# Kernel optimization log

Measured on AMD Instinct MI355X. Metric: run time of the kernel, lower is better.

The kernel has to match this reference:

```python
import jax, jax.numpy as jnp
import numpy as np

B, T, D = 2, 4096, 512
H = 8
HD = D // H  # 64


def setup_inputs() -> dict:
    key = jax.random.key(0)
    k1, k2, k3 = jax.random.split(key, 3)
    x = jax.random.normal(k1, (B, T, D), dtype=jnp.float32)
    w_qkv = jax.random.normal(k2, (3 * D, D), dtype=jnp.float32) * (1.0 / np.sqrt(D))
    w_out = jax.random.normal(k3, (D, D), dtype=jnp.float32) * (1.0 / np.sqrt(D))
    return {"x": x, "w_qkv": w_qkv, "w_out": w_out}


def reference(x, w_qkv, w_out):
    b, t, d = x.shape
    qkv = x @ w_qkv.T                      # [B,T,3D]
    q, k, v = jnp.split(qkv, 3, axis=-1)
    # b t (h d) -> b h t d
    def split_heads(a):
        return a.reshape(b, t, H, HD).transpose(0, 2, 1, 3)
    q, k, v = split_heads(q), split_heads(k), split_heads(v)
    scale = 1.0 / np.sqrt(HD).astype(np.float32)
    scores = jnp.einsum('bhqd,bhkd->bhqk', q, k) * scale  # [B,H,T,T]
    causal = jnp.tril(jnp.ones((t, t), dtype=bool))        # keep lower triangle
    scores = jnp.where(causal[None, None], scores, -jnp.inf)
    attn = jax.nn.softmax(scores, axis=-1)
    out = jnp.einsum('bhqk,bhkd->bhqd', attn, v)           # [B,H,T,HD]
    out = out.transpose(0, 2, 1, 3).reshape(b, t, d)       # b h t d -> b t (h d)
    return out @ w_out.T
```

## Files before the change

kernel.cpp:

```cpp
#include <hip/hip_runtime.h>
#include <hip/hip_bf16.h>

#define BB 2
#define TT 4096
#define DD 512
#define HH 8
#define HD 64
#define M_TOT (BB*TT)
#define N_QKV (3*DD)

typedef __attribute__((ext_vector_type(8))) __bf16 bf16x8;
typedef __attribute__((ext_vector_type(4))) float f32x4;

#define MFMA32(a,b,c) __builtin_amdgcn_mfma_f32_16x16x32_bf16((a),(b),(c),0,0,0)

#define SCALE_L2E 0.18033688011112443f
#define SHIFT_L2E 11.541560327111707f

static __device__ __forceinline__ unsigned short f2bf(float f) {
    union { float f; unsigned u; } v; v.f = f;
    return (unsigned short)((v.u + 0x8000u) >> 16);
}
static __device__ __forceinline__ unsigned short f2bf_t(float f) {
    union { float f; unsigned u; } v; v.f = f;
    return (unsigned short)(v.u >> 16);
}

static __device__ __forceinline__ bf16x8 load8(const unsigned short* p) {
    bf16x8 v;
    __builtin_memcpy(&v, p, 16);
    return v;
}

static __device__ __forceinline__ bf16x8 ones_frag() {
    unsigned short u[8];
    #pragma unroll
    for (int i = 0; i < 8; i++) u[i] = 0x3F80;
    bf16x8 v; __builtin_memcpy(&v, u, 16);
    return v;
}

#define GLDS(gp, lp) __builtin_amdgcn_global_load_lds( \
    (const __attribute__((address_space(1))) unsigned int*)(gp), \
    (__attribute__((address_space(3))) unsigned int*)(lp), 16, 0, 0)

#define NX4 (M_TOT*DD/4)
#define NW4 (N_QKV*DD/4)
#define NO4 (DD*DD/4)
__global__ __launch_bounds__(256) void cast_all(
        const float* __restrict__ x, const float* __restrict__ wqkv,
        const float* __restrict__ wout,
        unsigned short* __restrict__ xb, unsigned short* __restrict__ wqkvb,
        unsigned short* __restrict__ woutb) {
    int i = blockIdx.x * 256 + threadIdx.x;
    const float* s; unsigned short* d; int j;
    if (i < NX4)            { s = x;    d = xb;    j = i; }
    else if (i < NX4 + NW4) { s = wqkv; d = wqkvb; j = i - NX4; }
    else                    { s = wout; d = woutb; j = i - NX4 - NW4; }
    float4 f = ((const float4*)s)[j];
    ushort4 o;
    o.x = f2bf(f.x); o.y = f2bf(f.y); o.z = f2bf(f.z); o.w = f2bf(f.w);
    ((ushort4*)d)[j] = o;
}

__global__ __launch_bounds__(256) void qkv_gemm(
        const unsigned short* __restrict__ xb,
        const unsigned short* __restrict__ wb,
        unsigned short* __restrict__ qb,
        unsigned short* __restrict__ kb,
        unsigned short* __restrict__ vtb) {
    __shared__ union {
        struct { unsigned short As[128 * 32]; unsigned short Bs[128 * 32]; } g;
        unsigned short vt[4][64][72];
    } sm;
    int tid = threadIdx.x;
    int w = tid >> 6, lane = tid & 63;
    int lrow = lane & 15, quad = lane >> 4;
    int bn = blockIdx.x % (N_QKV / 128);
    int bm = blockIdx.x / (N_QKV / 128);
    int m0 = bm * 128, n0 = bn * 128;
    int wm = w >> 1, wn = w & 1;

    f32x4 c[4][4];
    #pragma unroll
    for (int i = 0; i < 4; i++)
        #pragma unroll
        for (int j = 0; j < 4; j++) c[i][j] = (f32x4){0.f, 0.f, 0.f, 0.f};

    for (int k0 = 0; k0 < DD; k0 += 32) {
        #pragma unroll
        for (int j = 0; j < 2; j++) {
            int ch = j * 256 + tid;
            int row = ch >> 2, kc = ch & 3;
            GLDS(xb + (size_t)(m0 + row) * DD + k0 + kc * 8,
                 (char*)sm.g.As + (size_t)(j * 256 + w * 64) * 16);
        }
        #pragma unroll
        for (int j = 0; j < 2; j++) {
            int ch = j * 256 + tid;
            int row = ch >> 2, kc = ch & 3;
            GLDS(wb + (size_t)(n0 + row) * DD + k0 + kc * 8,
                 (char*)sm.g.Bs + (size_t)(j * 256 + w * 64) * 16);
        }
        __syncthreads();
        bf16x8 a[4], b[4];
        #pragma unroll
        for (int mf = 0; mf < 4; mf++) a[mf] = load8(&sm.g.As[(wm * 64 + mf * 16 + lrow) * 32 + quad * 8]);
        #pragma unroll
        for (int nf = 0; nf < 4; nf++) b[nf] = load8(&sm.g.Bs[(wn * 64 + nf * 16 + lrow) * 32 + quad * 8]);
        #pragma unroll
        for (int mf = 0; mf < 4; mf++)
            #pragma unroll
            for (int nf = 0; nf < 4; nf++)
                c[mf][nf] = MFMA32(a[mf], b[nf], c[mf][nf]);
        __syncthreads();
    }

    int m0w = m0 + wm * 64, n0w = n0 + wn * 64;
    int which = n0w >> 9;
    int h = (n0w & 511) >> 6;
    if (which < 2) {
        unsigned short* dst = (which == 0) ? qb : kb;
        #pragma unroll
        for (int mf = 0; mf < 4; mf++) {
            #pragma unroll
            for (int r = 0; r < 4; r++) {
                int m = m0w + mf * 16 + quad * 4 + r;
                int t = m & (TT - 1), bi = m >> 12;
                size_t hb = (size_t)(bi * HH + h) * TT + t;
                #pragma unroll
                for (int nf = 0; nf < 4; nf++)
                    dst[hb * HD + nf * 16 + lrow] = f2bf(c[mf][nf][r]);
            }
        }
    } else {
        #pragma unroll
        for (int mf = 0; mf < 4; mf++)
            #pragma unroll
            for (int r = 0; r < 4; r++)
                #pragma unroll
                for (int nf = 0; nf < 4; nf++)
                    sm.vt[w][nf * 16 + lrow][mf * 16 + quad * 4 + r] = f2bf(c[mf][nf][r]);
        int bi = m0w >> 12, t0 = m0w & (TT - 1);
        size_t hb = (size_t)(bi * HH + h) * HD;
        #pragma unroll
        for (int i = 0; i < 8; i++) {
            int d = i * 8 + (lane >> 3);
            int tc = (lane & 7) * 8;
            bf16x8 v;
            __builtin_memcpy(&v, &sm.vt[w][d][tc], 16);
            __builtin_memcpy(vtb + (hb + d) * TT + t0 + tc, &v, 16);
        }
    }
}

__global__ __launch_bounds__(256) void attn_kernel(
        const unsigned short* __restrict__ qb,
        const unsigned short* __restrict__ kb,
        const unsigned short* __restrict__ vtb,
        unsigned short* __restrict__ attnb) {
    __shared__ union {
        unsigned short p[4][64][68];
        float c[2][64][66];
    } sm;

    const f32x4 ZERO4 = {0.f, 0.f, 0.f, 0.f};
    int w = threadIdx.x >> 6;
    int lane = threadIdx.x & 63;
    int lrow = lane & 15, quad = lane >> 4;
    int bh = blockIdx.x & 15;
    int pr = blockIdx.x >> 4;
    int bi = bh >> 3, h = bh & 7;

    const unsigned short* qh = qb + (size_t)bh * TT * HD;
    const unsigned short* kh = kb + (size_t)bh * TT * HD;
    const unsigned short* vth = vtb + (size_t)bh * HD * TT;
    bf16x8 ones = ones_frag();

    for (int half = 0; half < 2; half++) {
        int qt = half ? (63 - pr) : pr;
        int q0 = qt * 64;

        bf16x8 qf[4][2];
        #pragma unroll
        for (int mf = 0; mf < 4; mf++) {
            const unsigned short* qp = qh + (q0 + mf * 16 + lrow) * HD + quad * 8;
            qf[mf][0] = load8(qp);
            qf[mf][1] = load8(qp + 32);
        }

        f32x4 o[4][4];
        f32x4 l[4];
        #pragma unroll
        for (int i = 0; i < 4; i++) {
            l[i] = ZERO4;
            #pragma unroll
            for (int j = 0; j < 4; j++) o[i][j] = ZERO4;
        }

        for (int kt = w; kt <= qt; kt += 4) {
            int kbase = kt * 64;
            bool diag = (kt == qt);
            bf16x8 kf[4][2], vf[4][2];
            #pragma unroll
            for (int nf = 0; nf < 4; nf++) {
                const unsigned short* kp = kh + (kbase + nf * 16 + lrow) * HD + quad * 8;
                kf[nf][0] = load8(kp);
                kf[nf][1] = load8(kp + 32);
                const unsigned short* vp = vth + (nf * 16 + lrow) * TT + kbase + quad * 8;
                vf[nf][0] = load8(vp);
                vf[nf][1] = load8(vp + 32);
            }
            #pragma unroll
            for (int mf = 0; mf < 4; mf++) {
                #pragma unroll
                for (int nf = 0; nf < 4; nf++) {
                    if (diag && nf > mf) {
                        #pragma unroll
                        for (int r = 0; r < 4; r++)
                            sm.p[w][mf * 16 + quad * 4 + r][nf * 16 + lrow] = 0;
                    } else {
                        f32x4 s = MFMA32(qf[mf][0], kf[nf][0], ZERO4);
                        s = MFMA32(qf[mf][1], kf[nf][1], s);
                        #pragma unroll
                        for (int r = 0; r < 4; r++) {
                            float p = __builtin_amdgcn_exp2f(s[r] * SCALE_L2E - SHIFT_L2E);
                            if (diag && nf == mf && lrow > quad * 4 + r) p = 0.f;
                            sm.p[w][mf * 16 + quad * 4 + r][nf * 16 + lrow] = f2bf_t(p);
                        }
                    }
                }
                bf16x8 pa0, pa1;
                __builtin_memcpy(&pa0, &sm.p[w][mf * 16 + lrow][quad * 8], 16);
                __builtin_memcpy(&pa1, &sm.p[w][mf * 16 + lrow][32 + quad * 8], 16);
                l[mf] = MFMA32(pa0, ones, l[mf]);
                l[mf] = MFMA32(pa1, ones, l[mf]);
                #pragma unroll
                for (int nfd = 0; nfd < 4; nfd++) {
                    o[mf][nfd] = MFMA32(pa0, vf[nfd][0], o[mf][nfd]);
                    o[mf][nfd] = MFMA32(pa1, vf[nfd][1], o[mf][nfd]);
                }
            }
        }

        __syncthreads();
        if (w >= 2) {
            int cb = w - 2;
            #pragma unroll
            for (int mf = 0; mf < 4; mf++)
                #pragma unroll
                for (int r = 0; r < 4; r++) {
                    int row = mf * 16 + quad * 4 + r;
                    #pragma unroll
                    for (int nfd = 0; nfd < 4; nfd++)
                        sm.c[cb][row][nfd * 16 + lrow] = o[mf][nfd][r];
                    if (lrow == 0) sm.c[cb][row][64] = l[mf][r];
                }
        }
        __syncthreads();
        if (w < 2) {
            #pragma unroll
            for (int mf = 0; mf < 4; mf++)
                #pragma unroll
                for (int r = 0; r < 4; r++) {
                    int row = mf * 16 + quad * 4 + r;
                    #pragma unroll
                    for (int nfd = 0; nfd < 4; nfd++)
                        sm.c[w][row][nfd * 16 + lrow] += o[mf][nfd][r];
                    if (lrow == 0) sm.c[w][row][64] += l[mf][r];
                }
        }
        __syncthreads();
        {
            int q = threadIdx.x >> 2, dseg = (threadIdx.x & 3) * 16;
            const float* r0 = &sm.c[0][q][0];
            const float* r1 = &sm.c[1][q][0];
            float inv = 1.0f / (r0[64] + r1[64]);
            unsigned outp[8];
            #pragma unroll
            for (int i = 0; i < 8; i++) {
                float a0 = (r0[dseg + 2 * i] + r1[dseg + 2 * i]) * inv;
                float a1 = (r0[dseg + 2 * i + 1] + r1[dseg + 2 * i + 1]) * inv;
                outp[i] = (unsigned)f2bf_t(a0) | ((unsigned)f2bf_t(a1) << 16);
            }
            unsigned short* dst = attnb + ((size_t)(bi * TT + q0 + q)) * DD + h * HD + dseg;
            __builtin_memcpy(dst, outp, 16);
            __builtin_memcpy(dst + 8, outp + 4, 16);
        }
        __syncthreads();
    }
}

__global__ __launch_bounds__(256) void proj_gemm(
        const unsigned short* __restrict__ ab,
        const unsigned short* __restrict__ wb,
        float* __restrict__ out) {
    __shared__ unsigned short As[64 * 32];
    __shared__ unsigned short Bs[128 * 32];
    int tid = threadIdx.x;
    int w = tid >> 6, lane = tid & 63;
    int lrow = lane & 15, quad = lane >> 4;
    int bn = blockIdx.x % (DD / 128);
    int bm = blockIdx.x / (DD / 128);
    int m0 = bm * 64, n0 = bn * 128;

    f32x4 c[4][2];
    #pragma unroll
    for (int i = 0; i < 4; i++)
        #pragma unroll
        for (int j = 0; j < 2; j++) c[i][j] = (f32x4){0.f, 0.f, 0.f, 0.f};

    for (int k0 = 0; k0 < DD; k0 += 32) {
        {
            int ch = tid;
            int row = ch >> 2, kc = ch & 3;
            GLDS(ab + (size_t)(m0 + row) * DD + k0 + kc * 8,
                 (char*)As + (size_t)(w * 64) * 16);
        }
        #pragma unroll
        for (int j = 0; j < 2; j++) {
            int ch = j * 256 + tid;
            int row = ch >> 2, kc = ch & 3;
            GLDS(wb + (size_t)(n0 + row) * DD + k0 + kc * 8,
                 (char*)Bs + (size_t)(j * 256 + w * 64) * 16);
        }
        __syncthreads();
        bf16x8 a[4], b[2];
        #pragma unroll
        for (int mf = 0; mf < 4; mf++) a[mf] = load8(&As[(mf * 16 + lrow) * 32 + quad * 8]);
        #pragma unroll
        for (int nf = 0; nf < 2; nf++) b[nf] = load8(&Bs[(w * 32 + nf * 16 + lrow) * 32 + quad * 8]);
        #pragma unroll
        for (int mf = 0; mf < 4; mf++)
            #pragma unroll
            for (int nf = 0; nf < 2; nf++)
                c[mf][nf] = MFMA32(a[mf], b[nf], c[mf][nf]);
        __syncthreads();
    }

    #pragma unroll
    for (int mf = 0; mf < 4; mf++) {
        #pragma unroll
        for (int r = 0; r < 4; r++) {
            int m = m0 + mf * 16 + quad * 4 + r;
            #pragma unroll
            for (int nf = 0; nf < 2; nf++) {
                int n = n0 + w * 32 + nf * 16 + lrow;
                out[(size_t)m * DD + n] = c[mf][nf][r];
            }
        }
    }
}

extern "C" void kernel_launch(void* const* d_in, const int* in_sizes, int n_in,
                              void* d_out, int out_size, void* d_ws, size_t ws_size,
                              hipStream_t stream) {
    const float* x    = (const float*)d_in[0];
    const float* wqkv = (const float*)d_in[1];
    const float* wout = (const float*)d_in[2];
    float* out = (float*)d_out;

    char* ws = (char*)d_ws;
    unsigned short* xb    = (unsigned short*)ws; ws += (size_t)M_TOT * DD * 2;
    unsigned short* wqkvb = (unsigned short*)ws; ws += (size_t)N_QKV * DD * 2;
    unsigned short* woutb = (unsigned short*)ws; ws += (size_t)DD * DD * 2;
    unsigned short* qb    = (unsigned short*)ws; ws += (size_t)BB * HH * TT * HD * 2;
    unsigned short* kb    = (unsigned short*)ws; ws += (size_t)BB * HH * TT * HD * 2;
    unsigned short* vtb   = (unsigned short*)ws; ws += (size_t)BB * HH * HD * TT * 2;
    unsigned short* attnb = (unsigned short*)ws; ws += (size_t)M_TOT * DD * 2;

    cast_all<<<(NX4 + NW4 + NO4) / 256, 256, 0, stream>>>(x, wqkv, wout, xb, wqkvb, woutb);

    qkv_gemm<<<(M_TOT / 128) * (N_QKV / 128), 256, 0, stream>>>(xb, wqkvb, qb, kb, vtb);

    attn_kernel<<<512, 256, 0, stream>>>(qb, kb, vtb, attnb);

    proj_gemm<<<(M_TOT / 64) * (DD / 128), 256, 0, stream>>>(attnb, woutb, out);
}
```

Baseline: 176.8 us.

## Fuse fp32-to-bf16 casts into GEMM loads and restructure attention P stores

Drops the separate cast kernel. The QKV and projection GEMMs now read fp32 inputs and weights directly, convert them to bf16 in registers, and write them into swizzled LDS tiles. This gives up the async global_load_lds path for register-staged loads. The attention kernel swaps the MFMA operand order so each lane writes packed 8-byte P rows, and it pads the P buffer. The aim is to save a launch and a full bf16 round trip through memory, and to reduce LDS bank conflicts. In exchange, the GEMMs re-read fp32 data at twice the bytes and lose the async copy.

```diff
diff --git a/kernel.cpp b/kernel.cpp
--- a/kernel.cpp
+++ b/kernel.cpp
@@ -17,6 +17,21 @@
 #define SCALE_L2E 0.18033688011112443f
 #define SHIFT_L2E 11.541560327111707f
 
+static __device__ __forceinline__ unsigned pack_hi16(unsigned lo_u, unsigned hi_u) {
+#if __has_builtin(__builtin_amdgcn_perm)
+    return __builtin_amdgcn_perm(hi_u, lo_u, 0x07060302u);
+#else
+    return (lo_u >> 16) | (hi_u & 0xffff0000u);
+#endif
+}
+static __device__ __forceinline__ unsigned bfpack2_t(float a, float b) {
+    union { float f; unsigned u; } x, y; x.f = a; y.f = b;
+    return pack_hi16(x.u, y.u);
+}
+static __device__ __forceinline__ unsigned bfpack2_r(float a, float b) {
+    union { float f; unsigned u; } x, y; x.f = a; y.f = b;
+    return pack_hi16(x.u + 0x8000u, y.u + 0x8000u);
+}
 static __device__ __forceinline__ unsigned short f2bf(float f) {
     union { float f; unsigned u; } v; v.f = f;
     return (unsigned short)((v.u + 0x8000u) >> 16);
@@ -40,32 +55,18 @@
     return v;
 }
 
-#define GLDS(gp, lp) __builtin_amdgcn_global_load_lds( \
-    (const __attribute__((address_space(1))) unsigned int*)(gp), \
-    (__attribute__((address_space(3))) unsigned int*)(lp), 16, 0, 0)
-
-#define NX4 (M_TOT*DD/4)
-#define NW4 (N_QKV*DD/4)
-#define NO4 (DD*DD/4)
-__global__ __launch_bounds__(256) void cast_all(
-        const float* __restrict__ x, const float* __restrict__ wqkv,
-        const float* __restrict__ wout,
-        unsigned short* __restrict__ xb, unsigned short* __restrict__ wqkvb,
-        unsigned short* __restrict__ woutb) {
-    int i = blockIdx.x * 256 + threadIdx.x;
-    const float* s; unsigned short* d; int j;
-    if (i < NX4)            { s = x;    d = xb;    j = i; }
-    else if (i < NX4 + NW4) { s = wqkv; d = wqkvb; j = i - NX4; }
-    else                    { s = wout; d = woutb; j = i - NX4 - NW4; }
-    float4 f = ((const float4*)s)[j];
-    ushort4 o;
-    o.x = f2bf(f.x); o.y = f2bf(f.y); o.z = f2bf(f.z); o.w = f2bf(f.w);
-    ((ushort4*)d)[j] = o;
+static __device__ __forceinline__ void pack16(const float4& a0, const float4& a1,
+                                              const float4& a2, const float4& a3,
+                                              unsigned* o) {
+    o[0] = bfpack2_r(a0.x, a0.y); o[1] = bfpack2_r(a0.z, a0.w);
+    o[2] = bfpack2_r(a1.x, a1.y); o[3] = bfpack2_r(a1.z, a1.w);
+    o[4] = bfpack2_r(a2.x, a2.y); o[5] = bfpack2_r(a2.z, a2.w);
+    o[6] = bfpack2_r(a3.x, a3.y); o[7] = bfpack2_r(a3.z, a3.w);
 }
 
 __global__ __launch_bounds__(256) void qkv_gemm(
-        const unsigned short* __restrict__ xb,
-        const unsigned short* __restrict__ wb,
+        const float* __restrict__ x,
+        const float* __restrict__ wqkv,
         unsigned short* __restrict__ qb,
         unsigned short* __restrict__ kb,
         unsigned short* __restrict__ vtb) {
@@ -80,6 +81,11 @@
     int bm = blockIdx.x / (N_QKV / 128);
     int m0 = bm * 128, n0 = bn * 128;
     int wm = w >> 1, wn = w & 1;
+    int srow = tid >> 1, shalf = tid & 1;
+    int srs = (srow >> 1) & 3;
+    int sc0 = (2 * shalf + srs) & 3;
+    int sc1 = (2 * shalf + 1 + srs) & 3;
+    int rs = (lrow >> 1) & 3;
 
     f32x4 c[4][4];
     #pragma unroll
@@ -88,26 +94,25 @@
         for (int j = 0; j < 4; j++) c[i][j] = (f32x4){0.f, 0.f, 0.f, 0.f};
 
     for (int k0 = 0; k0 < DD; k0 += 32) {
-        #pragma unroll
-        for (int j = 0; j < 2; j++) {
-            int ch = j * 256 + tid;
-            int row = ch >> 2, kc = ch & 3;
-            GLDS(xb + (size_t)(m0 + row) * DD + k0 + kc * 8,
-                 (char*)sm.g.As + (size_t)(j * 256 + w * 64) * 16);
-        }
-        #pragma unroll
-        for (int j = 0; j < 2; j++) {
-            int ch = j * 256 + tid;
-            int row = ch >> 2, kc = ch & 3;
-            GLDS(wb + (size_t)(n0 + row) * DD + k0 + kc * 8,
-                 (char*)sm.g.Bs + (size_t)(j * 256 + w * 64) * 16);
-        }
+        const float4* ax = (const float4*)(x + (size_t)(m0 + srow) * DD + k0 + shalf * 16);
+        const float4* bx = (const float4*)(wqkv + (size_t)(n0 + srow) * DD + k0 + shalf * 16);
+        float4 a0 = ax[0], a1 = ax[1], a2 = ax[2], a3 = ax[3];
+        float4 b0 = bx[0], b1 = bx[1], b2 = bx[2], b3 = bx[3];
+        unsigned ap[8], bp[8];
+        pack16(a0, a1, a2, a3, ap);
+        pack16(b0, b1, b2, b3, bp);
+        __builtin_memcpy(&sm.g.As[srow * 32 + sc0 * 8], &ap[0], 16);
+        __builtin_memcpy(&sm.g.As[srow * 32 + sc1 * 8], &ap[4], 16);
+        __builtin_memcpy(&sm.g.Bs[srow * 32 + sc0 * 8], &bp[0], 16);
+        __builtin_memcpy(&sm.g.Bs[srow * 32 + sc1 * 8], &bp[4], 16);
         __syncthreads();
         bf16x8 a[4], b[4];
         #pragma unroll
-        for (int mf = 0; mf < 4; mf++) a[mf] = load8(&sm.g.As[(wm * 64 + mf * 16 + lrow) * 32 + quad * 8]);
-        #pragma unroll
-        for (int nf = 0; nf < 4; nf++) b[nf] = load8(&sm.g.Bs[(wn * 64 + nf * 16 + lrow) * 32 + quad * 8]);
+        for (int mf = 0; mf < 4; mf++)
+            a[mf] = load8(&sm.g.As[(wm * 64 + mf * 16 + lrow) * 32 + ((quad + rs) & 3) * 8]);
+        #pragma unroll
+        for (int nf = 0; nf < 4; nf++)
+            b[nf] = load8(&sm.g.Bs[(wn * 64 + nf * 16 + lrow) * 32 + ((quad + rs) & 3) * 8]);
         #pragma unroll
         for (int mf = 0; mf < 4; mf++)
             #pragma unroll
@@ -160,7 +165,7 @@
         const unsigned short* __restrict__ vtb,
         unsigned short* __restrict__ attnb) {
     __shared__ union {
-        unsigned short p[4][64][68];
+        unsigned short p[4][64][72];
         float c[2][64][66];
     } sm;
 
@@ -181,12 +186,12 @@
         int qt = half ? (63 - pr) : pr;
         int q0 = qt * 64;
 
-        bf16x8 qf[4][2];
-        #pragma unroll
-        for (int mf = 0; mf < 4; mf++) {
-            const unsigned short* qp = qh + (q0 + mf * 16 + lrow) * HD + quad * 8;
-            qf[mf][0] = load8(qp);
-            qf[mf][1] = load8(qp + 32);
+        bf16x8 qB[4][2];
+        #pragma unroll
+        for (int qf = 0; qf < 4; qf++) {
+            const unsigned short* qp = qh + (q0 + qf * 16 + lrow) * HD + quad * 8;
+            qB[qf][0] = load8(qp);
+            qB[qf][1] = load8(qp + 32);
         }
 
         f32x4 o[4][4];
@@ -212,33 +217,39 @@
                 vf[nf][1] = load8(vp + 32);
             }
             #pragma unroll
-            for (int mf = 0; mf < 4; mf++) {
-                #pragma unroll
-                for (int nf = 0; nf < 4; nf++) {
-                    if (diag && nf > mf) {
-                        #pragma unroll
-                        for (int r = 0; r < 4; r++)
-                            sm.p[w][mf * 16 + quad * 4 + r][nf * 16 + lrow] = 0;
+            for (int qf = 0; qf < 4; qf++) {
+                #pragma unroll
+                for (int tf = 0; tf < 4; tf++) {
+                    unsigned d01[2];
+                    if (diag && tf > qf) {
+                        d01[0] = 0u; d01[1] = 0u;
                     } else {
-                        f32x4 s = MFMA32(qf[mf][0], kf[nf][0], ZERO4);
-                        s = MFMA32(qf[mf][1], kf[nf][1], s);
-                        #pragma unroll
-                        for (int r = 0; r < 4; r++) {
-                            float p = __builtin_amdgcn_exp2f(s[r] * SCALE_L2E - SHIFT_L2E);
-                            if (diag && nf == mf && lrow > quad * 4 + r) p = 0.f;
-                            sm.p[w][mf * 16 + quad * 4 + r][nf * 16 + lrow] = f2bf_t(p);
+                        f32x4 s = MFMA32(kf[tf][0], qB[qf][0], ZERO4);
+                        s = MFMA32(kf[tf][1], qB[qf][1], s);
+                        float p0 = __builtin_amdgcn_exp2f(s[0] * SCALE_L2E - SHIFT_L2E);
+                        float p1 = __builtin_amdgcn_exp2f(s[1] * SCALE_L2E - SHIFT_L2E);
+                        float p2 = __builtin_amdgcn_exp2f(s[2] * SCALE_L2E - SHIFT_L2E);
+                        float p3 = __builtin_amdgcn_exp2f(s[3] * SCALE_L2E - SHIFT_L2E);
+                        if (diag && tf == qf) {
+                            if (quad * 4 + 0 > lrow) p0 = 0.f;
+                            if (quad * 4 + 1 > lrow) p1 = 0.f;
+                            if (quad * 4 + 2 > lrow) p2 = 0.f;
+                            if (quad * 4 + 3 > lrow) p3 = 0.f;
                         }
+                        d01[0] = bfpack2_t(p0, p1);
+                        d01[1] = bfpack2_t(p2, p3);
                     }
+                    __builtin_memcpy(&sm.p[w][qf * 16 + lrow][tf * 16 + quad * 4], d01, 8);
                 }
                 bf16x8 pa0, pa1;
-                __builtin_memcpy(&pa0, &sm.p[w][mf * 16 + lrow][quad * 8], 16);
-                __builtin_memcpy(&pa1, &sm.p[w][mf * 16 + lrow][32 + quad * 8], 16);
-                l[mf] = MFMA32(pa0, ones, l[mf]);
-                l[mf] = MFMA32(pa1, ones, l[mf]);
+                __builtin_memcpy(&pa0, &sm.p[w][qf * 16 + lrow][quad * 8], 16);
+                __builtin_memcpy(&pa1, &sm.p[w][qf * 16 + lrow][32 + quad * 8], 16);
+                l[qf] = MFMA32(pa0, ones, l[qf]);
+                l[qf] = MFMA32(pa1, ones, l[qf]);
                 #pragma unroll
                 for (int nfd = 0; nfd < 4; nfd++) {
-                    o[mf][nfd] = MFMA32(pa0, vf[nfd][0], o[mf][nfd]);
-                    o[mf][nfd] = MFMA32(pa1, vf[nfd][1], o[mf][nfd]);
+                    o[qf][nfd] = MFMA32(pa0, vf[nfd][0], o[qf][nfd]);
+                    o[qf][nfd] = MFMA32(pa1, vf[nfd][1], o[qf][nfd]);
                 }
             }
         }
@@ -293,16 +304,21 @@
 
 __global__ __launch_bounds__(256) void proj_gemm(
         const unsigned short* __restrict__ ab,
-        const unsigned short* __restrict__ wb,
+        const float* __restrict__ wout,
         float* __restrict__ out) {
-    __shared__ unsigned short As[64 * 32];
-    __shared__ unsigned short Bs[128 * 32];
+    __shared__ struct { unsigned short As[64 * 32]; unsigned short Bs[128 * 32]; } sm;
     int tid = threadIdx.x;
     int w = tid >> 6, lane = tid & 63;
     int lrow = lane & 15, quad = lane >> 4;
     int bn = blockIdx.x % (DD / 128);
     int bm = blockIdx.x / (DD / 128);
     int m0 = bm * 64, n0 = bn * 128;
+    int arow = tid >> 2, aseg = tid & 3;
+    int ac = (aseg + ((arow >> 1) & 3)) & 3;
+    int brow = tid >> 1, bhalf = tid & 1;
+    int brs = (brow >> 1) & 3;
+    int bc0 = (2 * bhalf + brs) & 3, bc1 = (2 * bhalf + 1 + brs) & 3;
+    int rs = (lrow >> 1) & 3;
 
     f32x4 c[4][2];
     #pragma unroll
@@ -311,25 +327,23 @@
         for (int j = 0; j < 2; j++) c[i][j] = (f32x4){0.f, 0.f, 0.f, 0.f};
 
     for (int k0 = 0; k0 < DD; k0 += 32) {
-        {
-            int ch = tid;
-            int row = ch >> 2, kc = ch & 3;
-            GLDS(ab + (size_t)(m0 + row) * DD + k0 + kc * 8,
-                 (char*)As + (size_t)(w * 64) * 16);
-        }
-        #pragma unroll
-        for (int j = 0; j < 2; j++) {
-            int ch = j * 256 + tid;
-            int row = ch >> 2, kc = ch & 3;
-            GLDS(wb + (size_t)(n0 + row) * DD + k0 + kc * 8,
-                 (char*)Bs + (size_t)(j * 256 + w * 64) * 16);
-        }
+        unsigned short apx[8];
+        __builtin_memcpy(apx, ab + (size_t)(m0 + arow) * DD + k0 + aseg * 8, 16);
+        const float4* bx = (const float4*)(wout + (size_t)(n0 + brow) * DD + k0 + bhalf * 16);
+        float4 b0 = bx[0], b1 = bx[1], b2 = bx[2], b3 = bx[3];
+        unsigned bp[8];
+        pack16(b0, b1, b2, b3, bp);
+        __builtin_memcpy(&sm.As[arow * 32 + ac * 8], apx, 16);
+        __builtin_memcpy(&sm.Bs[brow * 32 + bc0 * 8], &bp[0], 16);
+        __builtin_memcpy(&sm.Bs[brow * 32 + bc1 * 8], &bp[4], 16);
         __syncthreads();
         bf16x8 a[4], b[2];
         #pragma unroll
-        for (int mf = 0; mf < 4; mf++) a[mf] = load8(&As[(mf * 16 + lrow) * 32 + quad * 8]);
-        #pragma unroll
-        for (int nf = 0; nf < 2; nf++) b[nf] = load8(&Bs[(w * 32 + nf * 16 + lrow) * 32 + quad * 8]);
+        for (int mf = 0; mf < 4; mf++)
+            a[mf] = load8(&sm.As[(mf * 16 + lrow) * 32 + ((quad + rs) & 3) * 8]);
+        #pragma unroll
+        for (int nf = 0; nf < 2; nf++)
+            b[nf] = load8(&sm.Bs[(w * 32 + nf * 16 + lrow) * 32 + ((quad + rs) & 3) * 8]);
         #pragma unroll
         for (int mf = 0; mf < 4; mf++)
             #pragma unroll
@@ -361,19 +375,14 @@
     float* out = (float*)d_out;
 
     char* ws = (char*)d_ws;
-    unsigned short* xb    = (unsigned short*)ws; ws += (size_t)M_TOT * DD * 2;
-    unsigned short* wqkvb = (unsigned short*)ws; ws += (size_t)N_QKV * DD * 2;
-    unsigned short* woutb = (unsigned short*)ws; ws += (size_t)DD * DD * 2;
     unsigned short* qb    = (unsigned short*)ws; ws += (size_t)BB * HH * TT * HD * 2;
     unsigned short* kb    = (unsigned short*)ws; ws += (size_t)BB * HH * TT * HD * 2;
     unsigned short* vtb   = (unsigned short*)ws; ws += (size_t)BB * HH * HD * TT * 2;
     unsigned short* attnb = (unsigned short*)ws; ws += (size_t)M_TOT * DD * 2;
 
-    cast_all<<<(NX4 + NW4 + NO4) / 256, 256, 0, stream>>>(x, wqkv, wout, xb, wqkvb, woutb);
-
-    qkv_gemm<<<(M_TOT / 128) * (N_QKV / 128), 256, 0, stream>>>(xb, wqkvb, qb, kb, vtb);
+    qkv_gemm<<<(M_TOT / 128) * (N_QKV / 128), 256, 0, stream>>>(x, wqkv, qb, kb, vtb);
 
     attn_kernel<<<512, 256, 0, stream>>>(qb, kb, vtb, attnb);
 
-    proj_gemm<<<(M_TOT / 64) * (DD / 128), 256, 0, stream>>>(attnb, woutb, out);
-}
+    proj_gemm<<<(M_TOT / 64) * (DD / 128), 256, 0, stream>>>(attnb, wout, out);
+}
```

After: 186.2 us. +5.3%, slower.
